# Kernel tuning notes

Hardware: AMD Instinct MI355X
Metric: run time of the kernel (lower is better)

The kernel has to match this reference:

```python
import jax, jax.numpy as jnp
import numpy as np

SCALE = 64 ** 0.5  # module hard-codes sqrt(64), independent of output_dim


def setup_inputs() -> dict:
    key = jax.random.key(0)
    kx, kw = jax.random.split(key)
    x = jax.random.normal(kx, (8, 2048, 768), dtype=jnp.float32)
    kernel = jax.random.normal(kw, (3, 768, 768), dtype=jnp.float32) * 0.02
    return {"x": x, "kernel": kernel}


def reference(x, kernel):
    # x: [b, s, d]; kernel: [3, d, o]
    q = jnp.einsum('bsd,do->bso', x, kernel[0])
    k = jnp.einsum('bsd,do->bso', x, kernel[1])
    v = jnp.einsum('bsd,do->bso', x, kernel[2])
    scores = jnp.einsum('bso,bto->bst', q, k) / SCALE  # [b, s, s]
    attn = jax.nn.softmax(scores, axis=-1)
    return jnp.einsum('bst,bto->bso', attn, v)
```

## Files before the change

kernel.cpp:

```cpp
#include <hip/hip_runtime.h>

typedef unsigned short u16;
typedef unsigned int   u32;
typedef unsigned long long u64;
typedef __bf16  bf16x8 __attribute__((ext_vector_type(8)));
typedef float   f32x4  __attribute__((ext_vector_type(4)));

__device__ __forceinline__ u16 f2bf(float f) {
  u32 u = __builtin_bit_cast(u32, f);
  u += 0x7FFFu + ((u >> 16) & 1u);
  return (u16)(u >> 16);
}
__device__ __forceinline__ u32 pack2(float lo, float hi) {
  return (u32)f2bf(lo) | ((u32)f2bf(hi) << 16);
}

__device__ __forceinline__ void gload_lds16(const u16* g, u16* l) {
  __builtin_amdgcn_global_load_lds((const __attribute__((address_space(1))) void*)g,
                                   (__attribute__((address_space(3))) void*)l,
                                   16, 0, 0);
}

__global__ __launch_bounds__(256) void prep(const float* __restrict__ x,
                                            const float* __restrict__ w,
                                            u16* __restrict__ Xb,
                                            u16* __restrict__ Wt) {
  if (blockIdx.z < 3) {
    if (blockIdx.x >= 12 || blockIdx.y >= 12) return;
    __shared__ u16 t[64][65];
    const float* iz = w + (size_t)blockIdx.z * 768 * 768;
    u16* oz = Wt + (size_t)blockIdx.z * 768 * 768;
    const int tx = threadIdx.x & 63, ty = threadIdx.x >> 6;
    const int r0 = blockIdx.y * 64, c0 = blockIdx.x * 64;
#pragma unroll
    for (int rr = ty; rr < 64; rr += 4)
      t[rr][tx] = f2bf(iz[(size_t)(r0 + rr) * 768 + c0 + tx]);
    __syncthreads();
#pragma unroll
    for (int rr = ty; rr < 64; rr += 4)
      oz[(size_t)(c0 + rr) * 768 + r0 + tx] = t[tx][rr];
  } else {
    const size_t lin = (size_t)(blockIdx.z - 3) * 256 + blockIdx.y * 16 + blockIdx.x;
    const size_t i = lin * 256 + threadIdx.x;
    const float4* in4 = (const float4*)x;
    float4 a = in4[2 * i], b = in4[2 * i + 1];
    uint4 o;
    o.x = pack2(a.x, a.y); o.y = pack2(a.z, a.w);
    o.z = pack2(b.x, b.y); o.w = pack2(b.z, b.w);
    ((uint4*)Xb)[i] = o;
  }
}

template <int MODE, typename CT>
__global__ __launch_bounds__(512, 2)
void gemm_bt(const u16* __restrict__ A, const u16* __restrict__ B,
             CT* __restrict__ C, int Kd, int lda, int ldb, int ldc,
             size_t strideA, size_t strideB, size_t strideC,
             float* __restrict__ lsum, u16* __restrict__ vtp) {
  __shared__ __align__(16) u16 sh[2][2][256 * 64];

  const u32 gx = gridDim.x, gy = gridDim.y;
  const u32 lin = blockIdx.x + gx * (blockIdx.y + gy * blockIdx.z);
  const u32 nblk = gx * gy * gridDim.z;
  const u32 newlin = (lin & 7u) * (nblk >> 3) + (lin >> 3);
  const u32 bx = newlin % gx;
  const u32 tmp = newlin / gx;
  const u32 by = tmp % gy;
  const u32 bz = tmp / gy;

  const u16* Az = A + (size_t)bz * strideA;
  const u16* Bz = B + (size_t)bz * strideB;
  const int m0 = by * 256;
  const int n0g = bx * 256;
  int n0 = n0g;
  int matrix = 0;
  CT* Cz;
  if (MODE == 3) {
    matrix = n0g / 768;
    Cz = C + (size_t)matrix * strideC;
    n0 = n0g % 768;
  } else {
    Cz = C + (size_t)bz * strideC;
  }

  const int tid = threadIdx.x;
  const int lane = tid & 63, wave = tid >> 6;
  const int wr = wave >> 2, wc = wave & 3;
  const int wm = wr * 128, wn = wc * 64;
  const int lr = lane & 15, quad = lane >> 4;
  const int sr = lane >> 3;
  const int sc = ((lane & 7) ^ sr) << 3;

  const u16* gA = Az + (size_t)m0 * lda;
  const u16* gB = Bz + (size_t)n0g * ldb;

  f32x4 acc[8][4] = {};
  const int NT = Kd >> 6;

  auto stage = [&](int buf, int k0) {
#pragma unroll
    for (int r = 0; r < 4; ++r) {
      const int rows = r * 64 + wave * 8;
      gload_lds16(gA + (size_t)(rows + sr) * lda + (k0 + sc), &sh[buf][0][rows * 64]);
      gload_lds16(gB + (size_t)(rows + sr) * ldb + (k0 + sc), &sh[buf][1][rows * 64]);
    }
  };

  stage(0, 0);
  asm volatile("s_waitcnt vmcnt(0)" ::: "memory");
  __builtin_amdgcn_s_barrier();

  for (int t = 0; t < NT; ++t) {
    const char* sAc = (const char*)sh[t & 1][0];
    const char* sBc = (const char*)sh[t & 1][1];
    bf16x8 bq[4][2];
#pragma unroll
    for (int p = 0; p < 4; ++p) {
      if (p == 0 && t + 1 < NT) stage((t + 1) & 1, (t + 1) << 6);
      bf16x8 aq[2][2];
#pragma unroll
      for (int mi = 0; mi < 2; ++mi)
#pragma unroll
        for (int kc = 0; kc < 2; ++kc)
          aq[mi][kc] = *(const bf16x8*)(sAc + (wm + (2 * p + mi) * 16 + lr) * 128 +
                                        ((((kc << 2) + quad) ^ (lr & 7)) << 4));
      if (p == 0) {
#pragma unroll
        for (int nt = 0; nt < 4; ++nt)
#pragma unroll
          for (int kc = 0; kc < 2; ++kc)
            bq[nt][kc] = *(const bf16x8*)(sBc + (wn + nt * 16 + lr) * 128 +
                                          ((((kc << 2) + quad) ^ (lr & 7)) << 4));
      }
      asm volatile("" ::: "memory");
      __builtin_amdgcn_s_barrier();
      asm volatile("s_waitcnt lgkmcnt(0)" ::: "memory");
      __builtin_amdgcn_sched_barrier(0);
      __builtin_amdgcn_s_setprio(1);
#pragma unroll
      for (int mi = 0; mi < 2; ++mi)
#pragma unroll
        for (int nt = 0; nt < 4; ++nt)
#pragma unroll
          for (int kc = 0; kc < 2; ++kc)
            acc[2 * p + mi][nt] = __builtin_amdgcn_mfma_f32_16x16x32_bf16(
                aq[mi][kc], bq[nt][kc], acc[2 * p + mi][nt], 0, 0, 0);
      __builtin_amdgcn_s_setprio(0);
      asm volatile("" ::: "memory");
      if (p < 3) __builtin_amdgcn_s_barrier();
    }
    asm volatile("s_waitcnt vmcnt(0)" ::: "memory");
    __builtin_amdgcn_s_barrier();
  }

  if (MODE == 1) {
    float* rowsum = (float*)sh;
    if (tid < 256) rowsum[tid] = 0.f;
    __syncthreads();
#pragma unroll
    for (int mt = 0; mt < 8; ++mt) {
#pragma unroll
      for (int i = 0; i < 4; ++i) {
        const int row_l = wm + mt * 16 + quad * 4 + i;
        CT* cp = Cz + (size_t)(m0 + row_l) * ldc + (n0 + wn + lr);
        float e[4], s = 0.f;
#pragma unroll
        for (int nt = 0; nt < 4; ++nt) {
          e[nt] = __expf(acc[mt][nt][i] * 0.125f);
          s += e[nt];
          cp[nt * 16] = f2bf(e[nt]);
        }
        s += __shfl_xor(s, 1);  s += __shfl_xor(s, 2);
        s += __shfl_xor(s, 4);  s += __shfl_xor(s, 8);
        if (lr == 0) atomicAdd(&rowsum[row_l], s);
      }
    }
    __syncthreads();
    if (tid < 256)
      lsum[(size_t)bx * 16384 + (size_t)bz * 2048 + m0 + tid] = rowsum[tid];
  } else if (MODE == 2) {
    float* rinv = (float*)sh;
    if (tid < 256) {
      float s = 0.f;
      const size_t base = (size_t)bz * 2048 + m0 + tid;
#pragma unroll
      for (int xt = 0; xt < 8; ++xt) s += lsum[(size_t)xt * 16384 + base];
      rinv[tid] = 1.0f / s;
    }
    __syncthreads();
#pragma unroll
    for (int mt = 0; mt < 8; ++mt) {
#pragma unroll
      for (int i = 0; i < 4; ++i) {
        const int row_l = wm + mt * 16 + quad * 4 + i;
        const float iv = rinv[row_l];
        CT* cp = Cz + (size_t)(m0 + row_l) * ldc + (n0 + wn + lr);
#pragma unroll
        for (int nt = 0; nt < 4; ++nt) cp[nt * 16] = acc[mt][nt][i] * iv;
      }
    }
  } else if (MODE == 3 && matrix == 2) {
    u16* T = &sh[0][0][0];
#pragma unroll
    for (int mt = 0; mt < 8; ++mt) {
      const int rg = wr * 32 + mt * 4 + quad;
#pragma unroll
      for (int nt = 0; nt < 4; ++nt) {
        const int col = wn + nt * 16 + lr;
        u64 v = (u64)f2bf(acc[mt][nt][0])
              | ((u64)f2bf(acc[mt][nt][1]) << 16)
              | ((u64)f2bf(acc[mt][nt][2]) << 32)
              | ((u64)f2bf(acc[mt][nt][3]) << 48);
        *(u64*)((char*)T + col * 512 + ((rg ^ (col & 63)) << 3)) = v;
      }
    }
    __syncthreads();
    const int b = m0 >> 11;
#pragma unroll 4
    for (int it = 0; it < 32; ++it) {
      const int col = it * 8 + wave;
#pragma unroll
      for (int h = 0; h < 2; ++h) {
        const int rg = h * 32 + (lane >> 1);
        const u32 val = *(const u32*)((const char*)T + col * 512 +
                                      ((rg ^ (col & 63)) << 3) + ((lane & 1) << 2));
        *(u32*)(vtp + ((size_t)b * 768 + n0 + col) * 2048 +
                (m0 & 2047) + h * 128 + (lane << 1)) = val;
      }
    }
  } else {
#pragma unroll
    for (int mt = 0; mt < 8; ++mt) {
#pragma unroll
      for (int i = 0; i < 4; ++i) {
        const int row_l = wm + mt * 16 + quad * 4 + i;
        CT* cp = Cz + (size_t)(m0 + row_l) * ldc + (n0 + wn + lr);
#pragma unroll
        for (int nt = 0; nt < 4; ++nt) cp[nt * 16] = f2bf(acc[mt][nt][i]);
      }
    }
  }
}

extern "C" void kernel_launch(void* const* d_in, const int* in_sizes, int n_in,
                              void* d_out, int out_size, void* d_ws, size_t ws_size,
                              hipStream_t stream) {
  const float* x = (const float*)d_in[0];
  const float* w = (const float*)d_in[1];
  float* out = (float*)d_out;
  char* ws = (char*)d_ws;

  const size_t NS = (size_t)16384 * 768;
  u16* Sc = (u16*)ws;
  u16* Xb = (u16*)ws;
  u16* Wt = (u16*)(ws + NS * 2);
  u16* Qm = (u16*)(ws + 67108864);
  float* Lpart = (float*)(ws + 117440512);
  u16* Vt = (u16*)(ws + 142606336);

  prep<<<dim3(16, 16, 27), 256, 0, stream>>>(x, w, Xb, Wt);
  gemm_bt<3, u16><<<dim3(9, 64, 1), 512, 0, stream>>>(
      Xb, Wt, Qm, 768, 768, 768, 768, (size_t)0, (size_t)0, NS, Lpart, Vt);
  gemm_bt<1, u16><<<dim3(8, 8, 8), 512, 0, stream>>>(
      Qm, Qm + NS, Sc, 768, 768, 768, 2048, (size_t)2048 * 768, (size_t)2048 * 768,
      (size_t)2048 * 2048, Lpart, nullptr);
  gemm_bt<2, float><<<dim3(3, 8, 8), 512, 0, stream>>>(
      Sc, Vt, out, 2048, 2048, 2048, 768, (size_t)2048 * 2048,
      (size_t)768 * 2048, (size_t)2048 * 768, Lpart, nullptr);
}
```

Before: 305.8 us.

## Stagger A/B tile loads across phases with partial vmcnt waits in GEMM mainloop

```diff
diff --git a/kernel.cpp b/kernel.cpp
--- a/kernel.cpp
+++ b/kernel.cpp
@@ -96,61 +96,129 @@
 
   f32x4 acc[8][4] = {};
   const int NT = Kd >> 6;
-
-  auto stage = [&](int buf, int k0) {
-#pragma unroll
-    for (int r = 0; r < 4; ++r) {
-      const int rows = r * 64 + wave * 8;
+  const int NIT = NT >> 1;
+
+  auto stageA = [&](int buf, int half, int k0) {
+#pragma unroll
+    for (int r = 0; r < 2; ++r) {
+      const int rows = half * 128 + r * 64 + wave * 8;
       gload_lds16(gA + (size_t)(rows + sr) * lda + (k0 + sc), &sh[buf][0][rows * 64]);
+    }
+  };
+  auto stageB = [&](int buf, int half, int k0) {
+#pragma unroll
+    for (int r = 0; r < 2; ++r) {
+      const int rows = half * 128 + r * 64 + wave * 8;
       gload_lds16(gB + (size_t)(rows + sr) * ldb + (k0 + sc), &sh[buf][1][rows * 64]);
     }
   };
 
-  stage(0, 0);
-  asm volatile("s_waitcnt vmcnt(0)" ::: "memory");
+  stageA(0, 0, 0); stageA(0, 1, 0);
+  stageB(0, 0, 0); stageB(0, 1, 0);
+  stageB(1, 0, 64); stageB(1, 1, 64);
+  asm volatile("s_waitcnt vmcnt(4)" ::: "memory");
   __builtin_amdgcn_s_barrier();
 
-  for (int t = 0; t < NT; ++t) {
-    const char* sAc = (const char*)sh[t & 1][0];
-    const char* sBc = (const char*)sh[t & 1][1];
-    bf16x8 bq[4][2];
-#pragma unroll
-    for (int p = 0; p < 4; ++p) {
-      if (p == 0 && t + 1 < NT) stage((t + 1) & 1, (t + 1) << 6);
-      bf16x8 aq[2][2];
-#pragma unroll
-      for (int mi = 0; mi < 2; ++mi)
-#pragma unroll
-        for (int kc = 0; kc < 2; ++kc)
-          aq[mi][kc] = *(const bf16x8*)(sAc + (wm + (2 * p + mi) * 16 + lr) * 128 +
-                                        ((((kc << 2) + quad) ^ (lr & 7)) << 4));
-      if (p == 0) {
-#pragma unroll
-        for (int nt = 0; nt < 4; ++nt)
+  for (int i = 0; i < NIT; ++i) {
+    const bool full = (i + 1 < NIT);
+    const int kA = (2 * i + 1) << 6;
+    const int kN = (2 * i + 2) << 6;
+    const int kB2 = (2 * i + 3) << 6;
+
+    {
+      const char* sAc = (const char*)sh[0][0];
+      const char* sBc = (const char*)sh[0][1];
+      bf16x8 bq[4][2];
+#pragma unroll
+      for (int p = 0; p < 4; ++p) {
+        bf16x8 aq[2][2];
+#pragma unroll
+        for (int mi = 0; mi < 2; ++mi)
 #pragma unroll
           for (int kc = 0; kc < 2; ++kc)
-            bq[nt][kc] = *(const bf16x8*)(sBc + (wn + nt * 16 + lr) * 128 +
+            aq[mi][kc] = *(const bf16x8*)(sAc + (wm + (2 * p + mi) * 16 + lr) * 128 +
                                           ((((kc << 2) + quad) ^ (lr & 7)) << 4));
-      }
-      asm volatile("" ::: "memory");
+        if (p == 0) {
+#pragma unroll
+          for (int nt = 0; nt < 4; ++nt)
+#pragma unroll
+            for (int kc = 0; kc < 2; ++kc)
+              bq[nt][kc] = *(const bf16x8*)(sBc + (wn + nt * 16 + lr) * 128 +
+                                            ((((kc << 2) + quad) ^ (lr & 7)) << 4));
+          stageA(1, 0, kA);
+        } else if (p == 1) {
+          stageA(1, 1, kA);
+        } else if (p == 2) {
+          if (full) stageB(0, 0, kN);
+        } else {
+          if (full) stageB(0, 1, kN);
+        }
+        __builtin_amdgcn_s_barrier();
+        asm volatile("s_waitcnt lgkmcnt(0)" ::: "memory");
+        __builtin_amdgcn_sched_barrier(0);
+        __builtin_amdgcn_s_setprio(1);
+#pragma unroll
+        for (int mi = 0; mi < 2; ++mi)
+#pragma unroll
+          for (int nt = 0; nt < 4; ++nt)
+#pragma unroll
+            for (int kc = 0; kc < 2; ++kc)
+              acc[2 * p + mi][nt] = __builtin_amdgcn_mfma_f32_16x16x32_bf16(
+                  aq[mi][kc], bq[nt][kc], acc[2 * p + mi][nt], 0, 0, 0);
+        __builtin_amdgcn_s_setprio(0);
+        if (p < 3) __builtin_amdgcn_s_barrier();
+      }
+      if (full) asm volatile("s_waitcnt vmcnt(4)" ::: "memory");
+      else      asm volatile("s_waitcnt vmcnt(0)" ::: "memory");
       __builtin_amdgcn_s_barrier();
-      asm volatile("s_waitcnt lgkmcnt(0)" ::: "memory");
-      __builtin_amdgcn_sched_barrier(0);
-      __builtin_amdgcn_s_setprio(1);
-#pragma unroll
-      for (int mi = 0; mi < 2; ++mi)
-#pragma unroll
-        for (int nt = 0; nt < 4; ++nt)
+    }
+
+    {
+      const char* sAc = (const char*)sh[1][0];
+      const char* sBc = (const char*)sh[1][1];
+      bf16x8 bq[4][2];
+#pragma unroll
+      for (int p = 0; p < 4; ++p) {
+        bf16x8 aq[2][2];
+#pragma unroll
+        for (int mi = 0; mi < 2; ++mi)
 #pragma unroll
           for (int kc = 0; kc < 2; ++kc)
-            acc[2 * p + mi][nt] = __builtin_amdgcn_mfma_f32_16x16x32_bf16(
-                aq[mi][kc], bq[nt][kc], acc[2 * p + mi][nt], 0, 0, 0);
-      __builtin_amdgcn_s_setprio(0);
-      asm volatile("" ::: "memory");
-      if (p < 3) __builtin_amdgcn_s_barrier();
-    }
-    asm volatile("s_waitcnt vmcnt(0)" ::: "memory");
-    __builtin_amdgcn_s_barrier();
+            aq[mi][kc] = *(const bf16x8*)(sAc + (wm + (2 * p + mi) * 16 + lr) * 128 +
+                                          ((((kc << 2) + quad) ^ (lr & 7)) << 4));
+        if (p == 0) {
+#pragma unroll
+          for (int nt = 0; nt < 4; ++nt)
+#pragma unroll
+            for (int kc = 0; kc < 2; ++kc)
+              bq[nt][kc] = *(const bf16x8*)(sBc + (wn + nt * 16 + lr) * 128 +
+                                            ((((kc << 2) + quad) ^ (lr & 7)) << 4));
+          if (full) stageA(0, 0, kN);
+        } else if (p == 1) {
+          if (full) stageA(0, 1, kN);
+        } else if (p == 2) {
+          if (full) stageB(1, 0, kB2);
+        } else {
+          if (full) stageB(1, 1, kB2);
+        }
+        __builtin_amdgcn_s_barrier();
+        asm volatile("s_waitcnt lgkmcnt(0)" ::: "memory");
+        __builtin_amdgcn_sched_barrier(0);
+        __builtin_amdgcn_s_setprio(1);
+#pragma unroll
+        for (int mi = 0; mi < 2; ++mi)
+#pragma unroll
+          for (int nt = 0; nt < 4; ++nt)
+#pragma unroll
+            for (int kc = 0; kc < 2; ++kc)
+              acc[2 * p + mi][nt] = __builtin_amdgcn_mfma_f32_16x16x32_bf16(
+                  aq[mi][kc], bq[nt][kc], acc[2 * p + mi][nt], 0, 0, 0);
+        __builtin_amdgcn_s_setprio(0);
+        if (p < 3) __builtin_amdgcn_s_barrier();
+      }
+      if (full) asm volatile("s_waitcnt vmcnt(4)" ::: "memory");
+      __builtin_amdgcn_s_barrier();
+    }
   }
 
   if (MODE == 1) {
```

After: 292.0 us. 1.05x faster.

## Deepen GEMM prefetch to two tiles and spread loads across phases

Applied to the files above, without the earlier changes.

```diff
diff --git a/kernel.cpp b/kernel.cpp
--- a/kernel.cpp
+++ b/kernel.cpp
@@ -57,7 +57,7 @@
              CT* __restrict__ C, int Kd, int lda, int ldb, int ldc,
              size_t strideA, size_t strideB, size_t strideC,
              float* __restrict__ lsum, u16* __restrict__ vtp) {
-  __shared__ __align__(16) u16 sh[2][2][256 * 64];
+  __shared__ __align__(16) u16 sh[5][256 * 64];
 
   const u32 gx = gridDim.x, gy = gridDim.y;
   const u32 lin = blockIdx.x + gx * (blockIdx.y + gy * blockIdx.z);
@@ -97,26 +97,37 @@
   f32x4 acc[8][4] = {};
   const int NT = Kd >> 6;
 
-  auto stage = [&](int buf, int k0) {
-#pragma unroll
-    for (int r = 0; r < 4; ++r) {
-      const int rows = r * 64 + wave * 8;
-      gload_lds16(gA + (size_t)(rows + sr) * lda + (k0 + sc), &sh[buf][0][rows * 64]);
-      gload_lds16(gB + (size_t)(rows + sr) * ldb + (k0 + sc), &sh[buf][1][rows * 64]);
+  auto stageA = [&](int buf, int half, int k0) {
+#pragma unroll
+    for (int r = 0; r < 2; ++r) {
+      const int rows = half * 128 + r * 64 + wave * 8;
+      gload_lds16(gA + (size_t)(rows + sr) * lda + (k0 + sc), &sh[buf][rows * 64]);
     }
   };
-
-  stage(0, 0);
-  asm volatile("s_waitcnt vmcnt(0)" ::: "memory");
+  auto stageB = [&](int buf, int half, int k0) {
+#pragma unroll
+    for (int r = 0; r < 2; ++r) {
+      const int rows = half * 128 + r * 64 + wave * 8;
+      gload_lds16(gB + (size_t)(rows + sr) * ldb + (k0 + sc), &sh[3 + buf][rows * 64]);
+    }
+  };
+
+  stageA(0, 0, 0);  stageA(0, 1, 0);
+  stageB(0, 0, 0);  stageB(0, 1, 0);
+  stageA(1, 0, 64); stageA(1, 1, 64);
+  stageB(1, 0, 64); stageB(1, 1, 64);
+  asm volatile("s_waitcnt vmcnt(8)" ::: "memory");
   __builtin_amdgcn_s_barrier();
 
+  int ab = 0, ab2 = 2;
   for (int t = 0; t < NT; ++t) {
-    const char* sAc = (const char*)sh[t & 1][0];
-    const char* sBc = (const char*)sh[t & 1][1];
+    const char* sAc = (const char*)sh[ab];
+    const char* sBc = (const char*)sh[3 + (t & 1)];
+    const bool pf = (t + 2 < NT);
+    const int kP = (t + 2) << 6;
     bf16x8 bq[4][2];
 #pragma unroll
     for (int p = 0; p < 4; ++p) {
-      if (p == 0 && t + 1 < NT) stage((t + 1) & 1, (t + 1) << 6);
       bf16x8 aq[2][2];
 #pragma unroll
       for (int mi = 0; mi < 2; ++mi)
@@ -131,8 +142,14 @@
           for (int kc = 0; kc < 2; ++kc)
             bq[nt][kc] = *(const bf16x8*)(sBc + (wn + nt * 16 + lr) * 128 +
                                           ((((kc << 2) + quad) ^ (lr & 7)) << 4));
-      }
-      asm volatile("" ::: "memory");
+        if (pf) stageA(ab2, 0, kP);
+      } else if (p == 1) {
+        if (pf) stageA(ab2, 1, kP);
+      } else if (p == 2) {
+        if (pf) stageB(t & 1, 0, kP);
+      } else {
+        if (pf) stageB(t & 1, 1, kP);
+      }
       __builtin_amdgcn_s_barrier();
       asm volatile("s_waitcnt lgkmcnt(0)" ::: "memory");
       __builtin_amdgcn_sched_barrier(0);
@@ -146,11 +163,13 @@
             acc[2 * p + mi][nt] = __builtin_amdgcn_mfma_f32_16x16x32_bf16(
                 aq[mi][kc], bq[nt][kc], acc[2 * p + mi][nt], 0, 0, 0);
       __builtin_amdgcn_s_setprio(0);
-      asm volatile("" ::: "memory");
       if (p < 3) __builtin_amdgcn_s_barrier();
     }
-    asm volatile("s_waitcnt vmcnt(0)" ::: "memory");
+    if (pf) asm volatile("s_waitcnt vmcnt(8)" ::: "memory");
+    else    asm volatile("s_waitcnt vmcnt(0)" ::: "memory");
     __builtin_amdgcn_s_barrier();
+    ab  = (ab  + 1 == 3) ? 0 : ab  + 1;
+    ab2 = (ab2 + 1 == 3) ? 0 : ab2 + 1;
   }
 
   if (MODE == 1) {
@@ -200,7 +219,7 @@
       }
     }
   } else if (MODE == 3 && matrix == 2) {
-    u16* T = &sh[0][0][0];
+    u16* T = &sh[0][0];
 #pragma unroll
     for (int mt = 0; mt < 8; ++mt) {
       const int rg = wr * 32 + mt * 4 + quad;
```

After: 296.2 us. 3.1% less time.
